# Performance work log

Measured on AMD Instinct MI355X. Metric: run time of the kernel, lower is better.

Reference implementation:

```python
import jax, jax.numpy as jnp
import numpy as np

HIDDEN = 512
HEADS = 8
PREFIX = 1  # prefix_size: rows >= PREFIX may not attend to cols < PREFIX (except causal tril already zeroed those only partially)


def setup_inputs() -> dict:
    key = jax.random.key(0)
    k1, k2, k3 = jax.random.split(key, 3)
    B, L, D = 2, 4096, HIDDEN
    x = jax.random.normal(k1, (B, L, D), dtype=jnp.float32)
    # torch Linear(hidden, 3*hidden): y = x @ W^T + b; we store W^T directly as [D, 3D]
    w_in = jax.random.normal(k2, (D, 3 * D), dtype=jnp.float32) * (1.0 / np.sqrt(D))
    b_in = jnp.zeros((3 * D,), dtype=jnp.float32)
    w_out = jax.random.normal(k3, (D, D), dtype=jnp.float32) * (1.0 / np.sqrt(D))
    b_out = jnp.zeros((D,), dtype=jnp.float32)
    return {"x": x, "w_in": w_in, "b_in": b_in, "w_out": w_out, "b_out": b_out}


def _prefix_causal_mask(L):
    # tril(ones) then zero out [prefix:, :prefix]
    m = jnp.tril(jnp.ones((L, L), dtype=bool))
    m = m.at[PREFIX:, :PREFIX].set(False)
    return m  # True = attend allowed


def reference(x, w_in, b_in, w_out, b_out):
    B, L, D = x.shape
    H, hd = HEADS, D // HEADS
    qkv = x @ w_in + b_in  # [B, L, 3D]
    q, k, v = jnp.split(qkv, 3, axis=-1)
    q = q.reshape(B, L, H, hd).transpose(0, 2, 1, 3)  # [B,H,L,hd]
    k = k.reshape(B, L, H, hd).transpose(0, 2, 1, 3)
    v = v.reshape(B, L, H, hd).transpose(0, 2, 1, 3)
    scale = 1.0 / np.sqrt(hd).astype(np.float32)
    attn = jnp.einsum('bhqd,bhkd->bhqk', q, k) * scale  # [B,H,L,L]
    mask = _prefix_causal_mask(L)
    attn = jnp.where(mask[None, None, :, :], attn, -jnp.inf)
    attn = jax.nn.softmax(attn, axis=-1)  # dropout p=0.0 -> identity
    out = jnp.einsum('bhqk,bhkd->bhqd', attn, v)  # [B,H,L,hd]
    out = out.transpose(0, 2, 1, 3).reshape(B, L, D)
    return out @ w_out + b_out
```

## Files before the change

kernel.cpp:

```cpp
#include <hip/hip_runtime.h>
#include <hip/hip_bf16.h>

#define BSZ   2
#define LSEQ  4096
#define DH    512
#define NH    8
#define HDIM  64

typedef unsigned short ushort_t;
typedef __attribute__((ext_vector_type(8))) short s8v;
typedef __attribute__((ext_vector_type(4))) float f4v;

__device__ __forceinline__ ushort_t f2bf(float f) {
    __hip_bfloat16 h = __float2bfloat16(f);
    return *(ushort_t*)&h;
}

__device__ __forceinline__ void gld_lds16(const ushort_t* g, ushort_t* l) {
    __builtin_amdgcn_global_load_lds(
        (const __attribute__((address_space(1))) void*)g,
        (__attribute__((address_space(3))) void*)l, 16, 0, 0);
}

__device__ __forceinline__ void transpose_tile(const float* __restrict__ src,
                                               ushort_t* __restrict__ dst,
                                               int R, int C, int bx, int by)
{
    __shared__ float tile[32][33];
    int r0 = by * 32, c0 = bx * 32;
    int t = threadIdx.x;
    int tr = t >> 5, tc = t & 31;
    #pragma unroll
    for (int i = 0; i < 4; i++)
        tile[tr + 8 * i][tc] = src[(size_t)(r0 + tr + 8 * i) * C + c0 + tc];
    __syncthreads();
    #pragma unroll
    for (int i = 0; i < 4; i++) {
        int oc = tr + 8 * i;
        dst[(size_t)(c0 + oc) * R + r0 + tc] = f2bf(tile[tc][oc]);
    }
}

__global__ __launch_bounds__(256) void prep(const float* __restrict__ x,
                                            ushort_t* __restrict__ xb,
                                            const float* __restrict__ w_in,
                                            ushort_t* __restrict__ w_inT,
                                            const float* __restrict__ w_out,
                                            ushort_t* __restrict__ w_outT,
                                            float* __restrict__ Oacc,
                                            float* __restrict__ lacc)
{
    int bx = blockIdx.x;
    if (bx < 4096) {
        int i = (bx * 256 + threadIdx.x) * 4;
        float4 v = *(const float4*)&x[i];
        ushort_t o[4] = {f2bf(v.x), f2bf(v.y), f2bf(v.z), f2bf(v.w)};
        *(uint2*)&xb[i] = *(uint2*)o;
    } else if (bx < 4864) {
        int idx = bx - 4096;
        transpose_tile(w_in, w_inT, DH, 3 * DH, idx % 48, idx / 48);
    } else if (bx < 5120) {
        int idx = bx - 4864;
        transpose_tile(w_out, w_outT, DH, DH, idx % 16, idx / 16);
    } else if (bx < 9216) {
        int i = ((bx - 5120) * 256 + threadIdx.x) * 4;
        float4 z = {0.f, 0.f, 0.f, 0.f};
        *(float4*)&Oacc[i] = z;
    } else {
        int i = ((bx - 9216) * 256 + threadIdx.x) * 4;
        float4 z = {0.f, 0.f, 0.f, 0.f};
        *(float4*)&lacc[i] = z;
    }
}

__global__ __launch_bounds__(256) void vtrans(const ushort_t* __restrict__ qkv,
                                              ushort_t* __restrict__ vt)
{
    __shared__ ushort_t T[64][72];
    const int lt = blockIdx.x, h = blockIdx.y, b = blockIdx.z;
    const int l0 = lt * 64;
    const int t = threadIdx.x;
    {
        int r = t >> 2, c = (t & 3) * 16;
        size_t g = ((size_t)(b * LSEQ + l0 + r)) * (3 * DH) + 2 * DH + h * HDIM + c;
        *(uint4*)&T[r][c]     = *(const uint4*)&qkv[g];
        *(uint4*)&T[r][c + 8] = *(const uint4*)&qkv[g + 8];
    }
    __syncthreads();
    {
        int d = t >> 2, cl = (t & 3) * 16;
        ushort_t tmp[16];
        #pragma unroll
        for (int j = 0; j < 16; j++) tmp[j] = T[cl + j][d];
        size_t g = ((size_t)((b * NH + h) * 64 + d)) * LSEQ + l0 + cl;
        *(uint4*)&vt[g]     = *(uint4*)&tmp[0];
        *(uint4*)&vt[g + 8] = *(uint4*)&tmp[8];
    }
}

template <typename OUT>
__global__ __launch_bounds__(256) void gemm_bt(const ushort_t* __restrict__ A,
                                               const ushort_t* __restrict__ Bt,
                                               const float* __restrict__ bias,
                                               OUT* __restrict__ C,
                                               int M, int N, int K)
{
    __shared__ ushort_t As[128 * 32];
    __shared__ ushort_t Bs[128 * 32];
    const int tid = threadIdx.x;
    const int row0 = blockIdx.y * 128, col0 = blockIdx.x * 128;
    const int wid = tid >> 6, lane = tid & 63;
    const int wm = wid >> 1, wn = wid & 1;
    const int quad = lane >> 4, ln = lane & 15;

    f4v acc[4][4] = {};

    const int srow = (lane >> 2);
    const int scol = (lane & 3) * 8;

    for (int k0 = 0; k0 < K; k0 += 32) {
        #pragma unroll
        for (int t = 0; t < 2; t++) {
            int chunk = wid * 2 + t;
            int r = chunk * 16 + srow;
            gld_lds16(&A[(size_t)(row0 + r) * K + k0 + scol], &As[chunk * 512]);
            gld_lds16(&Bt[(size_t)(col0 + r) * K + k0 + scol], &Bs[chunk * 512]);
        }
        __syncthreads();
        s8v af[4], bf[4];
        #pragma unroll
        for (int mt = 0; mt < 4; mt++)
            af[mt] = *(const s8v*)&As[(wm * 64 + mt * 16 + ln) * 32 + quad * 8];
        #pragma unroll
        for (int nt = 0; nt < 4; nt++)
            bf[nt] = *(const s8v*)&Bs[(wn * 64 + nt * 16 + ln) * 32 + quad * 8];
        #pragma unroll
        for (int mt = 0; mt < 4; mt++)
            #pragma unroll
            for (int nt = 0; nt < 4; nt++)
                acc[mt][nt] = __builtin_amdgcn_mfma_f32_16x16x32_bf16(
                    af[mt], bf[nt], acc[mt][nt], 0, 0, 0);
        __syncthreads();
    }

    #pragma unroll
    for (int mt = 0; mt < 4; mt++) {
        #pragma unroll
        for (int nt = 0; nt < 4; nt++) {
            int c = col0 + wn * 64 + nt * 16 + ln;
            float bv = bias[c];
            #pragma unroll
            for (int reg = 0; reg < 4; reg++) {
                int r = row0 + wm * 64 + mt * 16 + quad * 4 + reg;
                float v = acc[mt][nt][reg] + bv;
                if constexpr (sizeof(OUT) == 2)
                    C[(size_t)r * N + c] = (OUT)f2bf(v);
                else
                    C[(size_t)r * N + c] = v;
            }
        }
    }
}

__global__ __launch_bounds__(128) void flash_mfma(const ushort_t* __restrict__ qkv,
                                                  const ushort_t* __restrict__ vt,
                                                  float* __restrict__ Oacc,
                                                  float* __restrict__ lacc)
{
    __shared__ ushort_t Ks[64 * 72];
    __shared__ ushort_t Vs[64 * 72];
    __shared__ ushort_t Ps[64 * 72];

    const int p     = blockIdx.x >> 1;
    const int khalf = blockIdx.x & 1;
    const int h = blockIdx.y, b = blockIdx.z;
    const int tid = threadIdx.x;
    const int w = tid >> 6, lane = tid & 63;
    const int quad = lane >> 4, ln = lane & 15;

    const int sr = tid >> 1, sc = (tid & 1) * 32;
    const int ldsw = sr * 72 + sc;
    const size_t kstep = (size_t)64 * 3 * DH;
    const float C_EXP = 0.18033688011112042f;

    const int qts[2] = {63 - p, p};

    for (int ti = 0; ti < 2; ti++) {
        const int qt = qts[ti], q0 = qt * 64;
        const int qrow0 = q0 + w * 32;
        const int n = qt + 1;
        const int ktBeg = khalf ? ((n + 1) >> 1) : 0;
        const int ktEnd = khalf ? n : ((n + 1) >> 1);

        s8v qa[2][2];
        #pragma unroll
        for (int qg = 0; qg < 2; qg++) {
            const ushort_t* qrow = qkv
                + ((size_t)(b * LSEQ + qrow0 + qg * 16 + ln)) * (3 * DH) + h * HDIM;
            qa[qg][0] = *(const s8v*)(qrow + quad * 8);
            qa[qg][1] = *(const s8v*)(qrow + 32 + quad * 8);
        }

        float l_s[2] = {0.0f, 0.0f};
        f4v o_acc[2][4] = {};

        size_t gk = ((size_t)(b * LSEQ + ktBeg * 64 + sr)) * (3 * DH) + DH + h * HDIM + sc;
        size_t gv = ((size_t)((b * NH + h) * 64 + sr)) * LSEQ + ktBeg * 64 + sc;
        uint4 pk0 = *(const uint4*)&qkv[gk];
        uint4 pk1 = *(const uint4*)&qkv[gk + 8];
        uint4 pk2 = *(const uint4*)&qkv[gk + 16];
        uint4 pk3 = *(const uint4*)&qkv[gk + 24];
        uint4 pv0 = *(const uint4*)&vt[gv];
        uint4 pv1 = *(const uint4*)&vt[gv + 8];
        uint4 pv2 = *(const uint4*)&vt[gv + 16];
        uint4 pv3 = *(const uint4*)&vt[gv + 24];

        for (int kt = ktBeg; kt < ktEnd; kt++) {
            const int k0 = kt * 64;
            __syncthreads();
            *(uint4*)&Ks[ldsw]      = pk0;
            *(uint4*)&Ks[ldsw + 8]  = pk1;
            *(uint4*)&Ks[ldsw + 16] = pk2;
            *(uint4*)&Ks[ldsw + 24] = pk3;
            *(uint4*)&Vs[ldsw]      = pv0;
            *(uint4*)&Vs[ldsw + 8]  = pv1;
            *(uint4*)&Vs[ldsw + 16] = pv2;
            *(uint4*)&Vs[ldsw + 24] = pv3;
            if (kt + 1 < ktEnd) {
                gk += kstep; gv += 64;
                pk0 = *(const uint4*)&qkv[gk];
                pk1 = *(const uint4*)&qkv[gk + 8];
                pk2 = *(const uint4*)&qkv[gk + 16];
                pk3 = *(const uint4*)&qkv[gk + 24];
                pv0 = *(const uint4*)&vt[gv];
                pv1 = *(const uint4*)&vt[gv + 8];
                pv2 = *(const uint4*)&vt[gv + 16];
                pv3 = *(const uint4*)&vt[gv + 24];
            }
            __syncthreads();

            s8v kb[4][2], vb[4][2];
            #pragma unroll
            for (int nt = 0; nt < 4; nt++) {
                kb[nt][0] = *(const s8v*)&Ks[(nt * 16 + ln) * 72 + quad * 8];
                kb[nt][1] = *(const s8v*)&Ks[(nt * 16 + ln) * 72 + 32 + quad * 8];
            }
            #pragma unroll
            for (int dt = 0; dt < 4; dt++) {
                vb[dt][0] = *(const s8v*)&Vs[(dt * 16 + ln) * 72 + quad * 8];
                vb[dt][1] = *(const s8v*)&Vs[(dt * 16 + ln) * 72 + 32 + quad * 8];
            }

            #pragma unroll
            for (int qg = 0; qg < 2; qg++) {
                f4v s[4] = {};
                #pragma unroll
                for (int nt = 0; nt < 4; nt++) {
                    s[nt] = __builtin_amdgcn_mfma_f32_16x16x32_bf16(kb[nt][0], qa[qg][0], s[nt], 0, 0, 0);
                    s[nt] = __builtin_amdgcn_mfma_f32_16x16x32_bf16(kb[nt][1], qa[qg][1], s[nt], 0, 0, 0);
                }

                float pp[4][4];
                const int q = qrow0 + qg * 16 + ln;
                if (kt == qt) {
                    #pragma unroll
                    for (int nt = 0; nt < 4; nt++) {
                        #pragma unroll
                        for (int reg = 0; reg < 4; reg++) {
                            int kidx = k0 + nt * 16 + quad * 4 + reg;
                            bool valid = (kidx <= q) && (kidx >= 1 || q == 0);
                            pp[nt][reg] = valid ? __builtin_amdgcn_exp2f(s[nt][reg] * C_EXP) : 0.0f;
                        }
                    }
                } else {
                    #pragma unroll
                    for (int nt = 0; nt < 4; nt++)
                        #pragma unroll
                        for (int reg = 0; reg < 4; reg++)
                            pp[nt][reg] = __builtin_amdgcn_exp2f(s[nt][reg] * C_EXP);
                    if (kt == 0 && quad == 0)
                        pp[0][0] = 0.0f;
                }

                #pragma unroll
                for (int nt = 0; nt < 4; nt++)
                    l_s[qg] += (pp[nt][0] + pp[nt][1]) + (pp[nt][2] + pp[nt][3]);

                const int prow = (w * 32 + qg * 16 + ln) * 72;
                #pragma unroll
                for (int nt = 0; nt < 4; nt++) {
                    unsigned int lo = (unsigned int)f2bf(pp[nt][0]) | ((unsigned int)f2bf(pp[nt][1]) << 16);
                    unsigned int hi = (unsigned int)f2bf(pp[nt][2]) | ((unsigned int)f2bf(pp[nt][3]) << 16);
                    uint2 pkd; pkd.x = lo; pkd.y = hi;
                    *(uint2*)&Ps[prow + nt * 16 + quad * 4] = pkd;
                }

                s8v pa0 = *(const s8v*)&Ps[prow + quad * 8];
                s8v pa1 = *(const s8v*)&Ps[prow + 32 + quad * 8];
                #pragma unroll
                for (int dt = 0; dt < 4; dt++) {
                    o_acc[qg][dt] = __builtin_amdgcn_mfma_f32_16x16x32_bf16(pa0, vb[dt][0], o_acc[qg][dt], 0, 0, 0);
                    o_acc[qg][dt] = __builtin_amdgcn_mfma_f32_16x16x32_bf16(pa1, vb[dt][1], o_acc[qg][dt], 0, 0, 0);
                }
            }
        }

        #pragma unroll
        for (int qg = 0; qg < 2; qg++) {
            float lf = l_s[qg];
            lf += __shfl_xor(lf, 16);
            lf += __shfl_xor(lf, 32);
            if (quad == 0)
                atomicAdd(&lacc[((size_t)(b * NH + h)) * LSEQ + qrow0 + qg * 16 + ln], lf);
            #pragma unroll
            for (int dt = 0; dt < 4; dt++)
                #pragma unroll
                for (int reg = 0; reg < 4; reg++)
                    atomicAdd(&Oacc[((size_t)(b * LSEQ + qrow0 + qg * 16 + quad * 4 + reg)) * DH
                                    + h * HDIM + dt * 16 + ln],
                              o_acc[qg][dt][reg]);
        }
    }
}

__global__ __launch_bounds__(256) void normalize(const float* __restrict__ Oacc,
                                                 const float* __restrict__ lacc,
                                                 ushort_t* __restrict__ att)
{
    int t = blockIdx.x * 256 + threadIdx.x;
    int row = t >> 5;
    int col0 = (t & 31) * 16;
    int h = col0 >> 6;
    int b = row >> 12, l = row & (LSEQ - 1);
    float linv = 1.0f / lacc[((size_t)(b * NH + h)) * LSEQ + l];
    const float* o = &Oacc[(size_t)row * DH + col0];
    ushort_t tmp[16];
    #pragma unroll
    for (int j = 0; j < 16; j++) tmp[j] = f2bf(o[j] * linv);
    size_t g = (size_t)row * DH + col0;
    *(uint4*)&att[g]     = *(uint4*)&tmp[0];
    *(uint4*)&att[g + 8] = *(uint4*)&tmp[8];
}

extern "C" void kernel_launch(void* const* d_in, const int* in_sizes, int n_in,
                              void* d_out, int out_size, void* d_ws, size_t ws_size,
                              hipStream_t stream)
{
    const float* x     = (const float*)d_in[0];
    const float* w_in  = (const float*)d_in[1];
    const float* b_in  = (const float*)d_in[2];
    const float* w_out = (const float*)d_in[3];
    const float* b_out = (const float*)d_in[4];
    float* out = (float*)d_out;

    const int M = BSZ * LSEQ;
    char* ws = (char*)d_ws;
    ushort_t* xb    = (ushort_t*)ws;                       ws += (size_t)M * DH * 2;
    ushort_t* w_inT = (ushort_t*)ws;                       ws += (size_t)3 * DH * DH * 2;
    ushort_t* w_outT= (ushort_t*)ws;                       ws += (size_t)DH * DH * 2;
    ushort_t* qkvb  = (ushort_t*)ws;                       ws += (size_t)M * 3 * DH * 2;
    ushort_t* vtb   = (ushort_t*)ws;                       ws += (size_t)M * DH * 2;
    ushort_t* attb  = (ushort_t*)ws;                       ws += (size_t)M * DH * 2;
    float*    Oacc  = (float*)ws;                          ws += (size_t)M * DH * 4;
    float*    lacc  = (float*)ws;

    prep<<<9280, 256, 0, stream>>>(x, xb, w_in, w_inT, w_out, w_outT, Oacc, lacc);

    gemm_bt<ushort_t><<<dim3(3 * DH / 128, M / 128), 256, 0, stream>>>(
        xb, w_inT, b_in, qkvb, M, 3 * DH, DH);

    vtrans<<<dim3(LSEQ / 64, NH, BSZ), 256, 0, stream>>>(qkvb, vtb);

    flash_mfma<<<dim3(64, NH, BSZ), 128, 0, stream>>>(qkvb, vtb, Oacc, lacc);

    normalize<<<1024, 256, 0, stream>>>(Oacc, lacc, attb);

    gemm_bt<float><<<dim3(DH / 128, M / 128), 256, 0, stream>>>(
        attb, w_outT, b_out, out, M, DH, DH);
}
```

Baseline: 194.6 us.

## Fuse V transpose and Q scaling into QKV GEMM; keep P in registers

The QKV projection GEMM epilogue now writes V directly in transposed layout and pre-multiplies Q by the softmax exp2 scale, so the separate vtrans kernel is gone and the per-element multiply leaves the flash loop. In the flash kernel, the P tile no longer round-trips through LDS. The MFMA accumulator layout of S is fed straight into 16x16x16 bf16 MFMAs using V fragments read in a matching layout. This removes a kernel launch, an LDS write/read per tile and some VALU work, but uses twice as many smaller MFMA instructions for the PV product.

```diff
diff --git a/kernel.cpp b/kernel.cpp
--- a/kernel.cpp
+++ b/kernel.cpp
@@ -9,7 +9,10 @@
 
 typedef unsigned short ushort_t;
 typedef __attribute__((ext_vector_type(8))) short s8v;
+typedef __attribute__((ext_vector_type(4))) short s4v;
 typedef __attribute__((ext_vector_type(4))) float f4v;
+
+#define C_EXP 0.18033688011112042f
 
 __device__ __forceinline__ ushort_t f2bf(float f) {
     __hip_bfloat16 h = __float2bfloat16(f);
@@ -73,36 +76,12 @@
     }
 }
 
-__global__ __launch_bounds__(256) void vtrans(const ushort_t* __restrict__ qkv,
-                                              ushort_t* __restrict__ vt)
-{
-    __shared__ ushort_t T[64][72];
-    const int lt = blockIdx.x, h = blockIdx.y, b = blockIdx.z;
-    const int l0 = lt * 64;
-    const int t = threadIdx.x;
-    {
-        int r = t >> 2, c = (t & 3) * 16;
-        size_t g = ((size_t)(b * LSEQ + l0 + r)) * (3 * DH) + 2 * DH + h * HDIM + c;
-        *(uint4*)&T[r][c]     = *(const uint4*)&qkv[g];
-        *(uint4*)&T[r][c + 8] = *(const uint4*)&qkv[g + 8];
-    }
-    __syncthreads();
-    {
-        int d = t >> 2, cl = (t & 3) * 16;
-        ushort_t tmp[16];
-        #pragma unroll
-        for (int j = 0; j < 16; j++) tmp[j] = T[cl + j][d];
-        size_t g = ((size_t)((b * NH + h) * 64 + d)) * LSEQ + l0 + cl;
-        *(uint4*)&vt[g]     = *(uint4*)&tmp[0];
-        *(uint4*)&vt[g + 8] = *(uint4*)&tmp[8];
-    }
-}
-
-template <typename OUT>
+template <typename OUT, bool QSCALE, bool VTRANS>
 __global__ __launch_bounds__(256) void gemm_bt(const ushort_t* __restrict__ A,
                                                const ushort_t* __restrict__ Bt,
                                                const float* __restrict__ bias,
                                                OUT* __restrict__ C,
+                                               ushort_t* __restrict__ vtout,
                                                int M, int N, int K)
 {
     __shared__ ushort_t As[128 * 32];
@@ -149,14 +128,31 @@
         for (int nt = 0; nt < 4; nt++) {
             int c = col0 + wn * 64 + nt * 16 + ln;
             float bv = bias[c];
-            #pragma unroll
-            for (int reg = 0; reg < 4; reg++) {
-                int r = row0 + wm * 64 + mt * 16 + quad * 4 + reg;
-                float v = acc[mt][nt][reg] + bv;
-                if constexpr (sizeof(OUT) == 2)
-                    C[(size_t)r * N + c] = (OUT)f2bf(v);
-                else
-                    C[(size_t)r * N + c] = v;
+            float scl = 1.0f;
+            if constexpr (QSCALE) scl = (c < DH) ? C_EXP : 1.0f;
+            bool vcol = false;
+            if constexpr (VTRANS) vcol = (c >= 2 * DH);
+            if (vcol) {
+                int d = c - 2 * DH;
+                int hh = d >> 6, dd = d & 63;
+                int r0 = row0 + wm * 64 + mt * 16 + quad * 4;
+                int bb = r0 >> 12, l = r0 & (LSEQ - 1);
+                ushort_t tmp[4];
+                #pragma unroll
+                for (int reg = 0; reg < 4; reg++)
+                    tmp[reg] = f2bf(acc[mt][nt][reg] + bv);
+                *(uint2*)&vtout[((size_t)((bb * NH + hh) * 64 + dd)) * LSEQ + l]
+                    = *(uint2*)tmp;
+            } else {
+                #pragma unroll
+                for (int reg = 0; reg < 4; reg++) {
+                    int r = row0 + wm * 64 + mt * 16 + quad * 4 + reg;
+                    float v = (acc[mt][nt][reg] + bv) * scl;
+                    if constexpr (sizeof(OUT) == 2)
+                        C[(size_t)r * N + c] = (OUT)f2bf(v);
+                    else
+                        C[(size_t)r * N + c] = v;
+                }
             }
         }
     }
@@ -169,7 +165,6 @@
 {
     __shared__ ushort_t Ks[64 * 72];
     __shared__ ushort_t Vs[64 * 72];
-    __shared__ ushort_t Ps[64 * 72];
 
     const int p     = blockIdx.x >> 1;
     const int khalf = blockIdx.x & 1;
@@ -181,7 +176,6 @@
     const int sr = tid >> 1, sc = (tid & 1) * 32;
     const int ldsw = sr * 72 + sc;
     const size_t kstep = (size_t)64 * 3 * DH;
-    const float C_EXP = 0.18033688011112042f;
 
     const int qts[2] = {63 - p, p};
 
@@ -204,103 +198,99 @@
         float l_s[2] = {0.0f, 0.0f};
         f4v o_acc[2][4] = {};
 
-        size_t gk = ((size_t)(b * LSEQ + ktBeg * 64 + sr)) * (3 * DH) + DH + h * HDIM + sc;
-        size_t gv = ((size_t)((b * NH + h) * 64 + sr)) * LSEQ + ktBeg * 64 + sc;
-        uint4 pk0 = *(const uint4*)&qkv[gk];
-        uint4 pk1 = *(const uint4*)&qkv[gk + 8];
-        uint4 pk2 = *(const uint4*)&qkv[gk + 16];
-        uint4 pk3 = *(const uint4*)&qkv[gk + 24];
-        uint4 pv0 = *(const uint4*)&vt[gv];
-        uint4 pv1 = *(const uint4*)&vt[gv + 8];
-        uint4 pv2 = *(const uint4*)&vt[gv + 16];
-        uint4 pv3 = *(const uint4*)&vt[gv + 24];
-
-        for (int kt = ktBeg; kt < ktEnd; kt++) {
-            const int k0 = kt * 64;
-            __syncthreads();
-            *(uint4*)&Ks[ldsw]      = pk0;
-            *(uint4*)&Ks[ldsw + 8]  = pk1;
-            *(uint4*)&Ks[ldsw + 16] = pk2;
-            *(uint4*)&Ks[ldsw + 24] = pk3;
-            *(uint4*)&Vs[ldsw]      = pv0;
-            *(uint4*)&Vs[ldsw + 8]  = pv1;
-            *(uint4*)&Vs[ldsw + 16] = pv2;
-            *(uint4*)&Vs[ldsw + 24] = pv3;
-            if (kt + 1 < ktEnd) {
-                gk += kstep; gv += 64;
-                pk0 = *(const uint4*)&qkv[gk];
-                pk1 = *(const uint4*)&qkv[gk + 8];
-                pk2 = *(const uint4*)&qkv[gk + 16];
-                pk3 = *(const uint4*)&qkv[gk + 24];
-                pv0 = *(const uint4*)&vt[gv];
-                pv1 = *(const uint4*)&vt[gv + 8];
-                pv2 = *(const uint4*)&vt[gv + 16];
-                pv3 = *(const uint4*)&vt[gv + 24];
-            }
-            __syncthreads();
-
-            s8v kb[4][2], vb[4][2];
-            #pragma unroll
-            for (int nt = 0; nt < 4; nt++) {
-                kb[nt][0] = *(const s8v*)&Ks[(nt * 16 + ln) * 72 + quad * 8];
-                kb[nt][1] = *(const s8v*)&Ks[(nt * 16 + ln) * 72 + 32 + quad * 8];
-            }
-            #pragma unroll
-            for (int dt = 0; dt < 4; dt++) {
-                vb[dt][0] = *(const s8v*)&Vs[(dt * 16 + ln) * 72 + quad * 8];
-                vb[dt][1] = *(const s8v*)&Vs[(dt * 16 + ln) * 72 + 32 + quad * 8];
-            }
-
-            #pragma unroll
-            for (int qg = 0; qg < 2; qg++) {
-                f4v s[4] = {};
+        if (ktBeg < ktEnd) {
+            size_t gk = ((size_t)(b * LSEQ + ktBeg * 64 + sr)) * (3 * DH) + DH + h * HDIM + sc;
+            size_t gv = ((size_t)((b * NH + h) * 64 + sr)) * LSEQ + ktBeg * 64 + sc;
+            uint4 pk0 = *(const uint4*)&qkv[gk];
+            uint4 pk1 = *(const uint4*)&qkv[gk + 8];
+            uint4 pk2 = *(const uint4*)&qkv[gk + 16];
+            uint4 pk3 = *(const uint4*)&qkv[gk + 24];
+            uint4 pv0 = *(const uint4*)&vt[gv];
+            uint4 pv1 = *(const uint4*)&vt[gv + 8];
+            uint4 pv2 = *(const uint4*)&vt[gv + 16];
+            uint4 pv3 = *(const uint4*)&vt[gv + 24];
+
+            for (int kt = ktBeg; kt < ktEnd; kt++) {
+                const int k0 = kt * 64;
+                __syncthreads();
+                *(uint4*)&Ks[ldsw]      = pk0;
+                *(uint4*)&Ks[ldsw + 8]  = pk1;
+                *(uint4*)&Ks[ldsw + 16] = pk2;
+                *(uint4*)&Ks[ldsw + 24] = pk3;
+                *(uint4*)&Vs[ldsw]      = pv0;
+                *(uint4*)&Vs[ldsw + 8]  = pv1;
+                *(uint4*)&Vs[ldsw + 16] = pv2;
+                *(uint4*)&Vs[ldsw + 24] = pv3;
+                if (kt + 1 < ktEnd) {
+                    gk += kstep; gv += 64;
+                    pk0 = *(const uint4*)&qkv[gk];
+                    pk1 = *(const uint4*)&qkv[gk + 8];
+                    pk2 = *(const uint4*)&qkv[gk + 16];
+                    pk3 = *(const uint4*)&qkv[gk + 24];
+                    pv0 = *(const uint4*)&vt[gv];
+                    pv1 = *(const uint4*)&vt[gv + 8];
+                    pv2 = *(const uint4*)&vt[gv + 16];
+                    pv3 = *(const uint4*)&vt[gv + 24];
+                }
+                __syncthreads();
+
+                s8v kb[4][2];
                 #pragma unroll
                 for (int nt = 0; nt < 4; nt++) {
-                    s[nt] = __builtin_amdgcn_mfma_f32_16x16x32_bf16(kb[nt][0], qa[qg][0], s[nt], 0, 0, 0);
-                    s[nt] = __builtin_amdgcn_mfma_f32_16x16x32_bf16(kb[nt][1], qa[qg][1], s[nt], 0, 0, 0);
+                    kb[nt][0] = *(const s8v*)&Ks[(nt * 16 + ln) * 72 + quad * 8];
+                    kb[nt][1] = *(const s8v*)&Ks[(nt * 16 + ln) * 72 + 32 + quad * 8];
                 }
-
-                float pp[4][4];
-                const int q = qrow0 + qg * 16 + ln;
-                if (kt == qt) {
+                s4v vf[4][4];
+                #pragma unroll
+                for (int dt = 0; dt < 4; dt++)
+                    #pragma unroll
+                    for (int nt = 0; nt < 4; nt++)
+                        vf[dt][nt] = *(const s4v*)&Vs[(dt * 16 + ln) * 72 + nt * 16 + quad * 4];
+
+                #pragma unroll
+                for (int qg = 0; qg < 2; qg++) {
+                    f4v s[4] = {};
                     #pragma unroll
                     for (int nt = 0; nt < 4; nt++) {
+                        s[nt] = __builtin_amdgcn_mfma_f32_16x16x32_bf16(kb[nt][0], qa[qg][0], s[nt], 0, 0, 0);
+                        s[nt] = __builtin_amdgcn_mfma_f32_16x16x32_bf16(kb[nt][1], qa[qg][1], s[nt], 0, 0, 0);
+                    }
+
+                    float pp[4][4];
+                    const int q = qrow0 + qg * 16 + ln;
+                    if (kt == qt) {
                         #pragma unroll
-                        for (int reg = 0; reg < 4; reg++) {
-                            int kidx = k0 + nt * 16 + quad * 4 + reg;
-                            bool valid = (kidx <= q) && (kidx >= 1 || q == 0);
-                            pp[nt][reg] = valid ? __builtin_amdgcn_exp2f(s[nt][reg] * C_EXP) : 0.0f;
+                        for (int nt = 0; nt < 4; nt++) {
+                            #pragma unroll
+                            for (int reg = 0; reg < 4; reg++) {
+                                int kidx = k0 + nt * 16 + quad * 4 + reg;
+                                bool valid = (kidx <= q) && (kidx >= 1 || q == 0);
+                                pp[nt][reg] = valid ? __builtin_amdgcn_exp2f(s[nt][reg]) : 0.0f;
+                            }
                         }
+                    } else {
+                        #pragma unroll
+                        for (int nt = 0; nt < 4; nt++)
+                            #pragma unroll
+                            for (int reg = 0; reg < 4; reg++)
+                                pp[nt][reg] = __builtin_amdgcn_exp2f(s[nt][reg]);
+                        if (kt == 0 && quad == 0)
+                            pp[0][0] = 0.0f;
                     }
-                } else {
+
                     #pragma unroll
                     for (int nt = 0; nt < 4; nt++)
+                        l_s[qg] += (pp[nt][0] + pp[nt][1]) + (pp[nt][2] + pp[nt][3]);
+
+                    #pragma unroll
+                    for (int nt = 0; nt < 4; nt++) {
+                        s4v pf = { (short)f2bf(pp[nt][0]), (short)f2bf(pp[nt][1]),
+                                   (short)f2bf(pp[nt][2]), (short)f2bf(pp[nt][3]) };
                         #pragma unroll
-                        for (int reg = 0; reg < 4; reg++)
-                            pp[nt][reg] = __builtin_amdgcn_exp2f(s[nt][reg] * C_EXP);
-                    if (kt == 0 && quad == 0)
-                        pp[0][0] = 0.0f;
-                }
-
-                #pragma unroll
-                for (int nt = 0; nt < 4; nt++)
-                    l_s[qg] += (pp[nt][0] + pp[nt][1]) + (pp[nt][2] + pp[nt][3]);
-
-                const int prow = (w * 32 + qg * 16 + ln) * 72;
-                #pragma unroll
-                for (int nt = 0; nt < 4; nt++) {
-                    unsigned int lo = (unsigned int)f2bf(pp[nt][0]) | ((unsigned int)f2bf(pp[nt][1]) << 16);
-                    unsigned int hi = (unsigned int)f2bf(pp[nt][2]) | ((unsigned int)f2bf(pp[nt][3]) << 16);
-                    uint2 pkd; pkd.x = lo; pkd.y = hi;
-                    *(uint2*)&Ps[prow + nt * 16 + quad * 4] = pkd;
-                }
-
-                s8v pa0 = *(const s8v*)&Ps[prow + quad * 8];
-                s8v pa1 = *(const s8v*)&Ps[prow + 32 + quad * 8];
-                #pragma unroll
-                for (int dt = 0; dt < 4; dt++) {
-                    o_acc[qg][dt] = __builtin_amdgcn_mfma_f32_16x16x32_bf16(pa0, vb[dt][0], o_acc[qg][dt], 0, 0, 0);
-                    o_acc[qg][dt] = __builtin_amdgcn_mfma_f32_16x16x32_bf16(pa1, vb[dt][1], o_acc[qg][dt], 0, 0, 0);
+                        for (int dt = 0; dt < 4; dt++)
+                            o_acc[qg][dt] = __builtin_amdgcn_mfma_f32_16x16x16bf16_1k(
+                                pf, vf[dt][nt], o_acc[qg][dt], 0, 0, 0);
+                    }
                 }
             }
         }
@@ -366,15 +356,13 @@
 
     prep<<<9280, 256, 0, stream>>>(x, xb, w_in, w_inT, w_out, w_outT, Oacc, lacc);
 
-    gemm_bt<ushort_t><<<dim3(3 * DH / 128, M / 128), 256, 0, stream>>>(
-        xb, w_inT, b_in, qkvb, M, 3 * DH, DH);
-
-    vtrans<<<dim3(LSEQ / 64, NH, BSZ), 256, 0, stream>>>(qkvb, vtb);
+    gemm_bt<ushort_t, true, true><<<dim3(3 * DH / 128, M / 128), 256, 0, stream>>>(
+        xb, w_inT, b_in, qkvb, vtb, M, 3 * DH, DH);
 
     flash_mfma<<<dim3(64, NH, BSZ), 128, 0, stream>>>(qkvb, vtb, Oacc, lacc);
 
     normalize<<<1024, 256, 0, stream>>>(Oacc, lacc, attb);
 
-    gemm_bt<float><<<dim3(DH / 128, M / 128), 256, 0, stream>>>(
-        attb, w_outT, b_out, out, M, DH, DH);
-}
+    gemm_bt<float, false, false><<<dim3(DH / 128, M / 128), 256, 0, stream>>>(
+        attb, w_outT, b_out, out, nullptr, M, DH, DH);
+}
```

After: 189.6 us. 2.6% less time.
